# Kernel optimization log

Measured on AMD Instinct MI355X. Metric: run time of the kernel, lower is better.

The kernel has to match this reference:

```python
import jax, jax.numpy as jnp
import numpy as np

BS = 128            # block_size
R, C = 4096, 2048   # weight shape (divisible by BS -> no padding needed)
NBR, NBC = R // BS, C // BS
NB = NBR * NBC      # 512 blocks
NUM_BITS = 4
NBINS = 2 * (2 ** NUM_BITS) - 1   # 31, from cat([-scaled.flip(0), scaled[1:]])
T = 100.0
A = 0.5
EPS = 1e-6


def _power_bins():
    lin = jnp.linspace(0.0, 1.0, 2 ** NUM_BITS)
    scaled = lin ** (1.0 / A) * 0.5
    return 0.5 + jnp.concatenate([-scaled[::-1], scaled[1:]])  # [NBINS]


def _to_blocks(w):
    # [R,C] -> [NB, BS, BS], row-major block order matching the torch double loop
    return w.reshape(NBR, BS, NBC, BS).transpose(0, 2, 1, 3).reshape(NB, BS, BS)


def _from_blocks(b):
    return b.reshape(NBR, NBC, BS, BS).transpose(0, 2, 1, 3).reshape(R, C)


def setup_inputs() -> dict:
    key = jax.random.key(0)
    weight = jax.random.normal(key, (R, C), dtype=jnp.float32) * 0.02
    blocks = _to_blocks(weight)
    bmin = blocks.min(axis=(1, 2))
    bmax = blocks.max(axis=(1, 2))
    pad = 0.05 * (bmax - bmin)
    w_min = bmin - pad                                  # [NB]
    w_max = bmax + pad                                  # [NB]
    bins = jnp.tile(_power_bins()[None, :], (NB, 1))    # [NB, NBINS]
    return {"weight": weight, "w_min": w_min, "w_max": w_max, "bins": bins}


def reference(weight, w_min, w_max, bins):
    blocks = _to_blocks(weight)  # [NB, BS, BS]
    # clamp bounds are detached in torch (.item()), replicate with stop_gradient
    wmin = jnp.minimum(w_min, jax.lax.stop_gradient(w_max) - EPS)
    wmax = jnp.maximum(w_max, jax.lax.stop_gradient(wmin) + EPS)
    span = wmax - wmin                                     # [NB]
    w_norm = (blocks - wmin[:, None, None]) / (span[:, None, None] + EPS)
    # distances to learnable bins: [NB, BS, BS, NBINS]
    dists = -jnp.abs(w_norm[..., None] - bins[:, None, None, :])
    soft = jax.nn.softmax(dists * T, axis=-1)
    w_q = jnp.einsum('nijl,nl->nij', soft, bins)
    w_deq = w_q * span[:, None, None] + wmin[:, None, None]
    # entropy: torch sums only over dim=0 of each [BS,BS,NBINS] block
    bin_mass = soft.sum(axis=1)                            # [NB, BS, NBINS]
    bin_probs = bin_mass / (bin_mass.sum(axis=(1, 2), keepdims=True) + EPS)
    total_entropy = -(bin_probs * jnp.log(bin_probs + EPS)).sum()
    out = _from_blocks(w_deq)                              # [R, C]
    return out, total_entropy
```

## Files before the change

### kernel.cpp

```cpp
#include <hip/hip_runtime.h>


#define RR 4096
#define CC 2048
#define BSZ 128
#define NBC 16
#define NBINS 31
#define EPS 1e-6f

__global__ void __launch_bounds__(512)
bq_kernel(const float* __restrict__ weight,
          const float* __restrict__ w_min,
          const float* __restrict__ w_max,
          const float* __restrict__ bins,
          float* __restrict__ out,
          float* __restrict__ ent_out)
{
    const int n   = blockIdx.x;
    const int br  = n >> 4;
    const int bc  = n & 15;
    const int tid = threadIdx.x;
    const int j   = tid & (BSZ - 1);
    const int q   = tid >> 7;

    __shared__ float smass[BSZ][NBINS + 2];
    __shared__ float sred[BSZ];
    __shared__ float swred[8];
    __shared__ float stot;

    for (int idx = tid; idx < BSZ * (NBINS + 2); idx += 512)
        (&smass[0][0])[idx] = 0.0f;
    __syncthreads();

    const float wmn      = w_min[n];
    const float wmx      = w_max[n];
    const float wmin_c   = fminf(wmn, wmx - EPS);
    const float wmax_c   = fmaxf(wmx, wmin_c + EPS);
    const float span     = wmax_c - wmin_c;
    const float inv_span = 1.0f / (span + EPS);

    float b[NBINS];
#pragma unroll
    for (int l = 0; l < NBINS; ++l) b[l] = bins[n * NBINS + l];

    float mass[NBINS];
#pragma unroll
    for (int l = 0; l < NBINS; ++l) mass[l] = 0.0f;

    const size_t base = (size_t)(br * BSZ + q * 32) * CC + (size_t)bc * BSZ + j;
    const float* wp = weight + base;
    float*       op = out + base;

    const float nT = -100.0f;

    for (int i = 0; i < 32; ++i) {
        float w  = wp[(size_t)i * CC];
        float wn = (w - wmin_c) * inv_span;

        float ev[NBINS];
        float sacc[4] = {0.f, 0.f, 0.f, 0.f};
        float qacc[4] = {0.f, 0.f, 0.f, 0.f};
#pragma unroll
        for (int l = 0; l < NBINS; ++l) {
            float ad = fabsf(wn - b[l]);
            float e  = __expf(nT * ad);
            ev[l] = e;
            sacc[l & 3] += e;
            qacc[l & 3] = fmaf(e, b[l], qacc[l & 3]);
        }
        float sum  = (sacc[0] + sacc[1]) + (sacc[2] + sacc[3]);
        float wq   = (qacc[0] + qacc[1]) + (qacc[2] + qacc[3]);
        float rsum = 1.0f / sum;

        op[(size_t)i * CC] = fmaf(wq * rsum, span, wmin_c);

#pragma unroll
        for (int l = 0; l < NBINS; ++l)
            mass[l] = fmaf(ev[l], rsum, mass[l]);
    }

#pragma unroll
    for (int l = 0; l < NBINS; ++l)
        atomicAdd(&smass[j][l], mass[l]);
    __syncthreads();

    if (tid < BSZ) {
        float cs = 0.0f;
#pragma unroll
        for (int l = 0; l < NBINS; ++l) cs += smass[tid][l];
        sred[tid] = cs;
    }
    __syncthreads();

    if (tid < 64) {
        float v = sred[tid] + sred[tid + 64];
#pragma unroll
        for (int off = 32; off > 0; off >>= 1)
            v += __shfl_down(v, off);
        if (tid == 0) stot = v;
    }
    __syncthreads();

    float ent = 0.0f;
    if (tid < BSZ) {
        float rtot = 1.0f / (stot + EPS);
#pragma unroll
        for (int l = 0; l < NBINS; ++l) {
            float p = smass[tid][l] * rtot;
            ent += p * __logf(p + EPS);
        }
    }
    float v = ent;
#pragma unroll
    for (int off = 32; off > 0; off >>= 1)
        v += __shfl_down(v, off);
    if ((tid & 63) == 0) swred[tid >> 6] = v;
    __syncthreads();
    if (tid == 0) {
        float t = 0.0f;
#pragma unroll
        for (int k = 0; k < 8; ++k) t += swred[k];
        atomicAdd(ent_out, -t);
    }
}

extern "C" void kernel_launch(void* const* d_in, const int* in_sizes, int n_in,
                              void* d_out, int out_size, void* d_ws, size_t ws_size,
                              hipStream_t stream) {
    const float* weight = (const float*)d_in[0];
    const float* wmin_p = (const float*)d_in[1];
    const float* wmax_p = (const float*)d_in[2];
    const float* bins_p = (const float*)d_in[3];
    float* out = (float*)d_out;
    float* ent = out + (size_t)RR * CC;

    hipMemsetAsync(ent, 0, sizeof(float), stream);
    bq_kernel<<<dim3(512), dim3(512), 0, stream>>>(weight, wmin_p, wmax_p, bins_p, out, ent);
}
```

Measured before the change: 153.5 us.

## Factor soft-bin exponentials into per-block prefix tables, dropping per-bin exp loop

```diff
diff --git a/kernel.cpp b/kernel.cpp
--- a/kernel.cpp
+++ b/kernel.cpp
@@ -4,9 +4,9 @@
 #define RR 4096
 #define CC 2048
 #define BSZ 128
-#define NBC 16
 #define NBINS 31
 #define EPS 1e-6f
+#define TT 100.0f
 
 __global__ void __launch_bounds__(512)
 bq_kernel(const float* __restrict__ weight,
@@ -23,14 +23,18 @@
     const int j   = tid & (BSZ - 1);
     const int q   = tid >> 7;
 
-    __shared__ float smass[BSZ][NBINS + 2];
-    __shared__ float sred[BSZ];
-    __shared__ float swred[8];
-    __shared__ float stot;
+    __shared__ float sU[BSZ][33];
+    __shared__ float sV[BSZ][33];
+    __shared__ float4 stab[32];
+    __shared__ double dEp[32];
+    __shared__ double dEm[32];
+    __shared__ double sred[8];
+    __shared__ double stot;
 
-    for (int idx = tid; idx < BSZ * (NBINS + 2); idx += 512)
-        (&smass[0][0])[idx] = 0.0f;
-    __syncthreads();
+    for (int idx = tid; idx < BSZ * 33; idx += 512) {
+        (&sU[0][0])[idx] = 0.0f;
+        (&sV[0][0])[idx] = 0.0f;
+    }
 
     const float wmn      = w_min[n];
     const float wmx      = w_max[n];
@@ -38,89 +42,117 @@
     const float wmax_c   = fmaxf(wmx, wmin_c + EPS);
     const float span     = wmax_c - wmin_c;
     const float inv_span = 1.0f / (span + EPS);
+    const float c0       = -wmin_c * inv_span - 0.5f;
 
-    float b[NBINS];
+    float bsv[NBINS];
 #pragma unroll
-    for (int l = 0; l < NBINS; ++l) b[l] = bins[n * NBINS + l];
+    for (int l = 0; l < NBINS; ++l) bsv[l] = bins[n * NBINS + l] - 0.5f;
 
-    float mass[NBINS];
+    if (tid < 64) {
+        const int lane = tid;
+        double bl  = (lane < NBINS) ? (double)bins[n * NBINS + lane] : 0.0;
+        double bs  = bl - 0.5;
+        double Ep  = (lane < NBINS) ? exp( 100.0 * bs) : 0.0;
+        double Em  = (lane < NBINS) ? exp(-100.0 * bs) : 0.0;
+        double EpB = Ep * bl;
+        double EmB = Em * bl;
+        double iEp = Ep, iEm = Em, iEpB = EpB, iEmB = EmB;
 #pragma unroll
-    for (int l = 0; l < NBINS; ++l) mass[l] = 0.0f;
+        for (int d = 1; d < 32; d <<= 1) {
+            double a0 = __shfl_up(iEp, d);
+            double a1 = __shfl_up(iEm, d);
+            double a2 = __shfl_up(iEpB, d);
+            double a3 = __shfl_up(iEmB, d);
+            if (lane >= d) { iEp += a0; iEm += a1; iEpB += a2; iEmB += a3; }
+        }
+        double totEm  = __shfl(iEm, 31);
+        double totEmB = __shfl(iEmB, 31);
+        if (lane < 32) {
+            float P  = (float)(iEp  - Ep);
+            float S  = (float)(totEm  - iEm  + Em);
+            float PQ = (float)(iEpB - EpB);
+            float SQ = (float)(totEmB - iEmB + EmB);
+            stab[lane] = make_float4(P, S, PQ, SQ);
+            dEp[lane] = Ep;
+            dEm[lane] = Em;
+        }
+    }
+    __syncthreads();
 
-    const size_t base = (size_t)(br * BSZ + q * 32) * CC + (size_t)bc * BSZ + j;
+    const size_t base = (size_t)(br * BSZ + q * 32) * CC + (size_t)(bc * BSZ) + j;
     const float* wp = weight + base;
     float*       op = out + base;
 
-    const float nT = -100.0f;
-
+#pragma unroll 4
     for (int i = 0; i < 32; ++i) {
-        float w  = wp[(size_t)i * CC];
-        float wn = (w - wmin_c) * inv_span;
-
-        float ev[NBINS];
-        float sacc[4] = {0.f, 0.f, 0.f, 0.f};
-        float qacc[4] = {0.f, 0.f, 0.f, 0.f};
+        float w = wp[(size_t)i * CC];
+        float u = fmaf(w, inv_span, c0);
+        int kk = 0;
 #pragma unroll
-        for (int l = 0; l < NBINS; ++l) {
-            float ad = fabsf(wn - b[l]);
-            float e  = __expf(nT * ad);
-            ev[l] = e;
-            sacc[l & 3] += e;
-            qacc[l & 3] = fmaf(e, b[l], qacc[l & 3]);
-        }
-        float sum  = (sacc[0] + sacc[1]) + (sacc[2] + sacc[3]);
-        float wq   = (qacc[0] + qacc[1]) + (qacc[2] + qacc[3]);
-        float rsum = 1.0f / sum;
-
+        for (int l = 0; l < NBINS; ++l) kk += (u >= bsv[l]);
+        float em = __expf(-TT * u);
+        float ep = __builtin_amdgcn_rcpf(em);
+        float4 t = stab[kk];
+        float sum  = fmaf(em, t.x, ep * t.y);
+        float rsum = __builtin_amdgcn_rcpf(sum);
+        float wq   = fmaf(em, t.z, ep * t.w);
         op[(size_t)i * CC] = fmaf(wq * rsum, span, wmin_c);
-
-#pragma unroll
-        for (int l = 0; l < NBINS; ++l)
-            mass[l] = fmaf(ev[l], rsum, mass[l]);
-    }
-
-#pragma unroll
-    for (int l = 0; l < NBINS; ++l)
-        atomicAdd(&smass[j][l], mass[l]);
-    __syncthreads();
-
-    if (tid < BSZ) {
-        float cs = 0.0f;
-#pragma unroll
-        for (int l = 0; l < NBINS; ++l) cs += smass[tid][l];
-        sred[tid] = cs;
+        atomicAdd(&sU[j][kk], em * rsum);
+        atomicAdd(&sV[j][kk], ep * rsum);
     }
     __syncthreads();
 
-    if (tid < 64) {
-        float v = sred[tid] + sred[tid + 64];
+    double colsum = 0.0;
+    if (tid < BSZ) {
+        double sufU = (double)sU[tid][31];
 #pragma unroll
-        for (int off = 32; off > 0; off >>= 1)
-            v += __shfl_down(v, off);
-        if (tid == 0) stot = v;
+        for (int l = 30; l >= 0; --l) {
+            double Ul = (double)sU[tid][l];
+            sU[tid][l] = (float)(dEp[l] * sufU);
+            sufU += Ul;
+        }
+        double preV = (double)sV[tid][0];
+#pragma unroll
+        for (int l = 0; l < NBINS; ++l) {
+            double mass = (double)sU[tid][l] + dEm[l] * preV;
+            colsum += mass;
+            sU[tid][l] = (float)mass;
+            if (l < 30) preV += (double)sV[tid][l + 1];
+        }
+    }
+
+    double v = colsum;
+#pragma unroll
+    for (int off = 32; off > 0; off >>= 1) v += __shfl_down(v, off);
+    if ((tid & 63) == 0) sred[tid >> 6] = v;
+    __syncthreads();
+    if (tid == 0) {
+        double t = 0.0;
+#pragma unroll
+        for (int k = 0; k < 8; ++k) t += sred[k];
+        stot = t;
     }
     __syncthreads();
+    const double rtot = 1.0 / (stot + (double)EPS);
 
-    float ent = 0.0f;
+    double ent = 0.0;
     if (tid < BSZ) {
-        float rtot = 1.0f / (stot + EPS);
 #pragma unroll
         for (int l = 0; l < NBINS; ++l) {
-            float p = smass[tid][l] * rtot;
-            ent += p * __logf(p + EPS);
+            double p = (double)sU[tid][l] * rtot;
+            ent += p * log(p + (double)EPS);
         }
     }
-    float v = ent;
+    double e = ent;
 #pragma unroll
-    for (int off = 32; off > 0; off >>= 1)
-        v += __shfl_down(v, off);
-    if ((tid & 63) == 0) swred[tid >> 6] = v;
+    for (int off = 32; off > 0; off >>= 1) e += __shfl_down(e, off);
+    if ((tid & 63) == 0) sred[tid >> 6] = e;
     __syncthreads();
     if (tid == 0) {
-        float t = 0.0f;
+        double t = 0.0;
 #pragma unroll
-        for (int k = 0; k < 8; ++k) t += swred[k];
-        atomicAdd(ent_out, -t);
+        for (int k = 0; k < 8; ++k) t += sred[k];
+        atomicAdd(ent_out, (float)(-t));
     }
 }
 
```

New measurement: 183.0 us. 1.19x slower.
